# Optimization experiments

Hardware: AMD Instinct MI355X
Metric: run time of the kernel (lower is better)

## Reference

```python
import jax, jax.numpy as jnp
import numpy as np

DIM = 1024
HEADS = 16
HEAD_DIM = DIM // HEADS
MLP_HIDDEN = int(DIM * 0.7)  # 716
EPS = 1e-5


def _ln(x, g, b):
    m = jnp.mean(x, axis=-1, keepdims=True)
    v = jnp.mean(jnp.square(x - m), axis=-1, keepdims=True)
    return (x - m) * jax.lax.rsqrt(v + EPS) * g + b


def setup_inputs() -> dict:
    key = jax.random.key(0)
    ks = jax.random.split(key, 8)
    B, N = 4, 1024
    x = jax.random.normal(ks[0], (B, N, DIM), dtype=jnp.float32)
    s = 0.02
    return {
        "x": x,
        "norm_g": jnp.ones((DIM,), jnp.float32),
        "norm_b": jnp.zeros((DIM,), jnp.float32),
        "W1": jax.random.normal(ks[1], (DIM, 3 * DIM + MLP_HIDDEN), jnp.float32) * s,
        "b1": jnp.zeros((3 * DIM + MLP_HIDDEN,), jnp.float32),
        "qn_g": jnp.ones((HEAD_DIM,), jnp.float32),
        "qn_b": jnp.zeros((HEAD_DIM,), jnp.float32),
        "kn_g": jnp.ones((HEAD_DIM,), jnp.float32),
        "kn_b": jnp.zeros((HEAD_DIM,), jnp.float32),
        "projW": jax.random.normal(ks[2], (DIM, DIM), jnp.float32) * s,
        "projb": jnp.zeros((DIM,), jnp.float32),
        "mlpW": jax.random.normal(ks[3], (MLP_HIDDEN, DIM), jnp.float32) * s,  # mlp_bias=False
        "W2": jax.random.normal(ks[4], (2 * DIM, DIM), jnp.float32) * s,
        "b2": jnp.zeros((DIM,), jnp.float32),
        "ls_g": jnp.full((DIM,), 1e-5, jnp.float32),
    }


def reference(x, norm_g, norm_b, W1, b1, qn_g, qn_b, kn_g, kn_b,
              projW, projb, mlpW, W2, b2, ls_g):
    B, N, C = x.shape
    norm_x = _ln(x, norm_g, norm_b)
    f1 = norm_x @ W1 + b1  # (B, N, 3*dim + mlp_hidden)
    qkv, mlp_hidden = f1[..., :3 * DIM], f1[..., 3 * DIM:]
    # (B, N, 3, H, hd) -> (3, B, H, N, hd)
    qkv = qkv.reshape(B, N, 3, HEADS, HEAD_DIM).transpose(2, 0, 3, 1, 4)
    q, k, v = qkv[0], qkv[1], qkv[2]
    q = _ln(q, qn_g, qn_b)
    k = _ln(k, kn_g, kn_b)
    attn = jnp.einsum('bhnd,bhmd->bhnm', q, k) * (HEAD_DIM ** -0.5)
    attn = jax.nn.softmax(attn, axis=-1)
    xo = jnp.einsum('bhnm,bhmd->bhnd', attn, v)
    xo = xo.transpose(0, 2, 1, 3).reshape(B, N, DIM)
    attn_out = xo @ projW + projb
    mlp_out = jax.nn.gelu(mlp_hidden, approximate=False) @ mlpW  # no bias
    combined = jnp.concatenate([attn_out, mlp_out], axis=-1)
    out = x + (combined @ W2 + b2) * ls_g
    return out
```

## Files before the change

kernel.cpp:

```cpp
#include <hip/hip_runtime.h>
#include <cstdint>
#include <cstddef>

typedef unsigned short u16;
typedef unsigned char u8;
typedef __attribute__((ext_vector_type(8))) u16 u16x8;
typedef __attribute__((ext_vector_type(8))) __bf16 bf16x8;
typedef __attribute__((ext_vector_type(4))) float f32x4;
typedef __attribute__((ext_vector_type(16))) float f32x16;
typedef __attribute__((ext_vector_type(4))) int i32x4;
typedef __attribute__((ext_vector_type(8))) int i32x8;
typedef __attribute__((ext_vector_type(2))) int i32x2;

__device__ __forceinline__ u16 f2bf(float f) {
  unsigned u = __builtin_bit_cast(unsigned, f);
  return (u16)((u + 0x7FFFu + ((u >> 16) & 1u)) >> 16);
}
__device__ __forceinline__ float bf2f(u16 h) {
  return __builtin_bit_cast(float, (unsigned)h << 16);
}
__device__ __forceinline__ u8 f2fp8(float f) {
  return (u8)(__builtin_amdgcn_cvt_pk_fp8_f32(f, 0.f, 0, false) & 0xFF);
}
__device__ __forceinline__ f32x4 mfma16(u16x8 a, u16x8 b, f32x4 c) {
  return __builtin_amdgcn_mfma_f32_16x16x32_bf16(
      __builtin_bit_cast(bf16x8, a), __builtin_bit_cast(bf16x8, b), c, 0, 0, 0);
}
__device__ __forceinline__ f32x16 mfma32(u16x8 a, u16x8 b, f32x16 c) {
  return __builtin_amdgcn_mfma_f32_32x32x16_bf16(
      __builtin_bit_cast(bf16x8, a), __builtin_bit_cast(bf16x8, b), c, 0, 0, 0);
}
__device__ __forceinline__ unsigned cvtpk_bf16(float lo, float hi) {
  unsigned r;
  asm("v_cvt_pk_bf16_f32 %0, %1, %2" : "=v"(r) : "v"(lo), "v"(hi));
  return r;
}
__device__ __forceinline__ void plswap(unsigned& a, unsigned& b) {
  i32x2 r = __builtin_amdgcn_permlane32_swap((int)a, (int)b, false, false);
  a = (unsigned)r[0];
  b = (unsigned)r[1];
}
__device__ __forceinline__ void load_lds16(const void* g, void* l) {
  __builtin_amdgcn_global_load_lds(
      (const __attribute__((address_space(1))) void*)g,
      (__attribute__((address_space(3))) void*)l, 16, 0, 0);
}

__global__ __launch_bounds__(256) void k_pre(
    const float* __restrict__ W1, const float* __restrict__ projW,
    const float* __restrict__ mlpW, const float* __restrict__ W2,
    u8* __restrict__ W1t, u8* __restrict__ pWt, u8* __restrict__ mWt,
    u8* __restrict__ W2t, const float* __restrict__ x,
    const float* __restrict__ g, const float* __restrict__ b,
    u8* __restrict__ nx8) {
  __shared__ float t[32][33];
  __shared__ float red[8];
  const int L = blockIdx.x;
  const int tid = threadIdx.x;
  if (L < 7680) {
    const float* src;
    u8* dst;
    int R, C, dR, dC, bx, by;
    if (L < 3840) {
      src = W1; dst = W1t; R = 1024; C = 3788; dR = 1024; dC = 3840;
      bx = L % 120; by = L / 120;
    } else if (L < 4864) {
      int tq = L - 3840;
      src = projW; dst = pWt; R = 1024; C = 1024; dR = 1024; dC = 1024;
      bx = tq & 31; by = tq >> 5;
    } else if (L < 5632) {
      int tq = L - 4864;
      src = mlpW; dst = mWt; R = 716; C = 1024; dR = 768; dC = 1024;
      bx = tq & 31; by = tq >> 5;
    } else {
      int tq = L - 5632;
      src = W2; dst = W2t; R = 2048; C = 1024; dR = 2048; dC = 1024;
      bx = tq & 31; by = tq >> 5;
    }
    const int n0 = bx * 32, k0 = by * 32;
    const int tx = tid & 31, ty = tid >> 5;
#pragma unroll
    for (int j = 0; j < 4; ++j) {
      int kk = k0 + ty + 8 * j, nn = n0 + tx;
      float v = (kk < R && nn < C) ? src[(size_t)kk * C + nn] : 0.f;
      t[ty + 8 * j][tx] = v;
    }
    __syncthreads();
#pragma unroll
    for (int j = 0; j < 4; ++j) {
      int nn = n0 + ty + 8 * j, kk = k0 + tx;
      if (nn < dC && kk < dR) dst[(size_t)nn * dR + kk] = f2fp8(t[tx][ty + 8 * j]);
    }
  } else {
    const int row = L - 7680;
    float4 v = ((const float4*)(x + (size_t)row * 1024))[tid];
    float s = v.x + v.y + v.z + v.w;
    float ss = v.x * v.x + v.y * v.y + v.z * v.z + v.w * v.w;
#pragma unroll
    for (int off = 1; off < 64; off <<= 1) {
      s += __shfl_xor(s, off);
      ss += __shfl_xor(ss, off);
    }
    const int wid = tid >> 6, lane = tid & 63;
    if (lane == 0) { red[wid] = s; red[4 + wid] = ss; }
    __syncthreads();
    s = red[0] + red[1] + red[2] + red[3];
    ss = red[4] + red[5] + red[6] + red[7];
    const float mean = s * (1.f / 1024.f);
    const float var = ss * (1.f / 1024.f) - mean * mean;
    const float rstd = rsqrtf(var + 1e-5f);
    float4 gv = ((const float4*)g)[tid];
    float4 bv = ((const float4*)b)[tid];
    float y0 = (v.x - mean) * rstd * gv.x + bv.x;
    float y1 = (v.y - mean) * rstd * gv.y + bv.y;
    float y2 = (v.z - mean) * rstd * gv.z + bv.z;
    float y3 = (v.w - mean) * rstd * gv.w + bv.w;
    int pk = __builtin_amdgcn_cvt_pk_fp8_f32(y0, y1, 0, false);
    pk = __builtin_amdgcn_cvt_pk_fp8_f32(y2, y3, pk, true);
    ((int*)(nx8 + (size_t)row * 1024))[tid] = pk;
  }
}

__device__ __forceinline__ void gemm_fp8_core(const u8* __restrict__ A,
                                              const u8* __restrict__ B, int K,
                                              u8* Alds, u8* Blds,
                                              f32x16 (&acc)[2][2], int tid) {
  const int lane = tid & 63, wave = tid >> 6;
  const int h = lane >> 5, r32 = lane & 31;
  const int wrow = (wave >> 1) * 64, wcol = (wave & 1) * 64;
  const int srow0 = tid >> 2, spos = tid & 3;
  const int nk = K >> 6;
  auto STAGE = [&](int t, int bb) {
#pragma unroll
    for (int p = 0; p < 2; ++p) {
      const int row = p * 64 + srow0;
      const int c = spos ^ ((row >> 1) & 3);
      const size_t go = (size_t)row * K + (size_t)t * 64 + c * 16;
      load_lds16(A + go, Alds + bb * 8192 + (p * 256 + tid) * 16);
      load_lds16(B + go, Blds + bb * 8192 + (p * 256 + tid) * 16);
    }
  };
  STAGE(0, 0);
  STAGE(1, 1);
  asm volatile("s_waitcnt vmcnt(4)" ::: "memory");
  __builtin_amdgcn_s_barrier();
  int cur = 0;
  for (int kt = 0; kt < nk; ++kt) {
    const u8* Ac = Alds + cur * 8192;
    const u8* Bc = Blds + cur * 8192;
    i32x8 af[2], bf[2];
#pragma unroll
    for (int t = 0; t < 2; ++t) {
      {
        const int row = wrow + t * 32 + r32;
        const int sw = (row >> 1) & 3;
        i32x4 lo = *(const i32x4*)(Ac + row * 64 + ((2 * h) ^ sw) * 16);
        i32x4 hi = *(const i32x4*)(Ac + row * 64 + ((2 * h + 1) ^ sw) * 16);
        i32x8 a;
        a[0] = lo[0]; a[1] = lo[1]; a[2] = lo[2]; a[3] = lo[3];
        a[4] = hi[0]; a[5] = hi[1]; a[6] = hi[2]; a[7] = hi[3];
        af[t] = a;
      }
      {
        const int row = wcol + t * 32 + r32;
        const int sw = (row >> 1) & 3;
        i32x4 lo = *(const i32x4*)(Bc + row * 64 + ((2 * h) ^ sw) * 16);
        i32x4 hi = *(const i32x4*)(Bc + row * 64 + ((2 * h + 1) ^ sw) * 16);
        i32x8 b8;
        b8[0] = lo[0]; b8[1] = lo[1]; b8[2] = lo[2]; b8[3] = lo[3];
        b8[4] = hi[0]; b8[5] = hi[1]; b8[6] = hi[2]; b8[7] = hi[3];
        bf[t] = b8;
      }
    }
    if (kt + 2 < nk) STAGE(kt + 2, cur == 0 ? 2 : cur - 1);
#pragma unroll
    for (int i = 0; i < 2; ++i)
#pragma unroll
      for (int j = 0; j < 2; ++j)
        acc[i][j] = __builtin_amdgcn_mfma_scale_f32_32x32x64_f8f6f4(
            af[i], bf[j], acc[i][j], 0, 0, 0, 0x7F7F7F7F, 0, 0x7F7F7F7F);
    if (kt + 1 < nk) {
      if (kt + 2 < nk)
        asm volatile("s_waitcnt vmcnt(4)" ::: "memory");
      else
        asm volatile("s_waitcnt vmcnt(0)" ::: "memory");
      __builtin_amdgcn_s_barrier();
    }
    cur = (cur == 2) ? 0 : cur + 1;
  }
}

__device__ __forceinline__ void gemm_fp8_core64(const u8* __restrict__ A,
                                                const u8* __restrict__ B, int K,
                                                u8* Alds, u8* Blds,
                                                f32x16 (&acc)[2], int tid) {
  const int lane = tid & 63, wave = tid >> 6;
  const int h = lane >> 5, r32 = lane & 31;
  const int wrow = (wave >> 1) * 32, wcol = (wave & 1) * 64;
  const int nk = K >> 6;
  const int ra = tid >> 2, posa = tid & 3;
  const int ca = posa ^ ((ra >> 1) & 3);
  auto STAGE = [&](int t, int bb) {
    const size_t k0 = (size_t)t * 64;
    load_lds16(A + (size_t)ra * K + k0 + ca * 16, Alds + bb * 4096 + tid * 16);
#pragma unroll
    for (int p = 0; p < 2; ++p) {
      const int s = tid + 256 * p;
      const int r = s >> 2, pos = s & 3;
      const int c = pos ^ ((r >> 1) & 3);
      load_lds16(B + (size_t)r * K + k0 + c * 16, Blds + bb * 8192 + s * 16);
    }
  };
  STAGE(0, 0);
  STAGE(1, 1);
  asm volatile("s_waitcnt vmcnt(3)" ::: "memory");
  __builtin_amdgcn_s_barrier();
  int cur = 0;
  for (int kt = 0; kt < nk; ++kt) {
    const u8* Ac = Alds + cur * 4096;
    const u8* Bc = Blds + cur * 8192;
    i32x8 af, bf[2];
    {
      const int row = wrow + r32;
      const int sw = (row >> 1) & 3;
      i32x4 lo = *(const i32x4*)(Ac + row * 64 + ((2 * h) ^ sw) * 16);
      i32x4 hi = *(const i32x4*)(Ac + row * 64 + ((2 * h + 1) ^ sw) * 16);
      af[0] = lo[0]; af[1] = lo[1]; af[2] = lo[2]; af[3] = lo[3];
      af[4] = hi[0]; af[5] = hi[1]; af[6] = hi[2]; af[7] = hi[3];
    }
#pragma unroll
    for (int t = 0; t < 2; ++t) {
      const int row = wcol + t * 32 + r32;
      const int sw = (row >> 1) & 3;
      i32x4 lo = *(const i32x4*)(Bc + row * 64 + ((2 * h) ^ sw) * 16);
      i32x4 hi = *(const i32x4*)(Bc + row * 64 + ((2 * h + 1) ^ sw) * 16);
      i32x8 b8;
      b8[0] = lo[0]; b8[1] = lo[1]; b8[2] = lo[2]; b8[3] = lo[3];
      b8[4] = hi[0]; b8[5] = hi[1]; b8[6] = hi[2]; b8[7] = hi[3];
      bf[t] = b8;
    }
    if (kt + 2 < nk) STAGE(kt + 2, cur == 0 ? 2 : cur - 1);
#pragma unroll
    for (int j = 0; j < 2; ++j)
      acc[j] = __builtin_amdgcn_mfma_scale_f32_32x32x64_f8f6f4(
          af, bf[j], acc[j], 0, 0, 0, 0x7F7F7F7F, 0, 0x7F7F7F7F);
    if (kt + 1 < nk) {
      if (kt + 2 < nk)
        asm volatile("s_waitcnt vmcnt(3)" ::: "memory");
      else
        asm volatile("s_waitcnt vmcnt(0)" ::: "memory");
      __builtin_amdgcn_s_barrier();
    }
    cur = (cur == 2) ? 0 : cur + 1;
  }
}

__global__ __launch_bounds__(256) void k_gemm1(const u8* __restrict__ nx8,
                                               const u8* __restrict__ W1t,
                                               u16* __restrict__ f1,
                                               const float* __restrict__ b1) {
  __shared__ __align__(16) u8 Alds[3 * 128 * 64];
  __shared__ __align__(16) u8 Blds[3 * 128 * 64];
  const int tid = threadIdx.x, bm = blockIdx.y, bn = blockIdx.x;
  f32x16 acc[2][2];
#pragma unroll
  for (int i = 0; i < 2; ++i)
#pragma unroll
    for (int j = 0; j < 2; ++j)
#pragma unroll
      for (int r = 0; r < 16; ++r) acc[i][j][r] = 0.f;
  gemm_fp8_core(nx8 + (size_t)bm * 128 * 1024, W1t + (size_t)bn * 128 * 1024, 1024,
                Alds, Blds, acc, tid);
  const int lane = tid & 63, wave = tid >> 6;
  const int h = lane >> 5, r32 = lane & 31;
  const int wrow = (wave >> 1) * 64, wcol = (wave & 1) * 64;
#pragma unroll
  for (int i = 0; i < 2; ++i)
#pragma unroll
    for (int j = 0; j < 2; ++j) {
      const int col = bn * 128 + wcol + j * 32 + r32;
      const float bs = (col < 3788) ? b1[col] : 0.f;
#pragma unroll
      for (int r = 0; r < 16; ++r) {
        const int row = bm * 128 + wrow + i * 32 + 4 * h + (r & 3) + 8 * (r >> 2);
        f1[(size_t)row * 3840 + col] = f2bf(acc[i][j][r] + bs);
      }
    }
}

__global__ __launch_bounds__(256) void k_gemm_pm(
    const u8* __restrict__ xo, const u8* __restrict__ pWt,
    const u8* __restrict__ gel, const u8* __restrict__ mWt,
    u8* __restrict__ comb, const float* __restrict__ projb) {
  __shared__ __align__(16) u8 Alds[3 * 64 * 64];
  __shared__ __align__(16) u8 Blds[3 * 128 * 64];
  const int tid = threadIdx.x, bm = blockIdx.y, bnq = blockIdx.x;
  const u8* A;
  const u8* B;
  int K, colbase;
  const float* bias;
  if (bnq < 8) {
    A = xo + (size_t)bm * 64 * 1024;
    B = pWt + (size_t)bnq * 128 * 1024;
    K = 1024; colbase = bnq * 128; bias = projb;
  } else {
    A = gel + (size_t)bm * 64 * 768;
    B = mWt + (size_t)(bnq - 8) * 128 * 768;
    K = 768; colbase = 1024 + (bnq - 8) * 128; bias = nullptr;
  }
  f32x16 acc[2];
#pragma unroll
  for (int j = 0; j < 2; ++j)
#pragma unroll
    for (int r = 0; r < 16; ++r) acc[j][r] = 0.f;
  gemm_fp8_core64(A, B, K, Alds, Blds, acc, tid);
  const int lane = tid & 63, wave = tid >> 6;
  const int h = lane >> 5, r32 = lane & 31;
  const int wrow = (wave >> 1) * 32, wcol = (wave & 1) * 64;
#pragma unroll
  for (int j = 0; j < 2; ++j) {
    const int col = colbase + wcol + j * 32 + r32;
    const float bs = (bias != nullptr) ? bias[col] : 0.f;
#pragma unroll
    for (int r = 0; r < 16; ++r) {
      const int row = bm * 64 + wrow + 4 * h + (r & 3) + 8 * (r >> 2);
      comb[(size_t)row * 2048 + col] = f2fp8(acc[j][r] + bs);
    }
  }
}

__global__ __launch_bounds__(256) void k_gemm_fin(const u8* __restrict__ comb,
                                                  const u8* __restrict__ W2t,
                                                  float* __restrict__ out,
                                                  const float* __restrict__ b2,
                                                  const float* __restrict__ x,
                                                  const float* __restrict__ lsg) {
  __shared__ __align__(16) u8 Alds[3 * 64 * 64];
  __shared__ __align__(16) u8 Blds[3 * 128 * 64];
  const int tid = threadIdx.x, bm = blockIdx.y, bn = blockIdx.x;
  f32x16 acc[2];
#pragma unroll
  for (int j = 0; j < 2; ++j)
#pragma unroll
    for (int r = 0; r < 16; ++r) acc[j][r] = 0.f;
  gemm_fp8_core64(comb + (size_t)bm * 64 * 2048, W2t + (size_t)bn * 128 * 2048, 2048,
                  Alds, Blds, acc, tid);
  const int lane = tid & 63, wave = tid >> 6;
  const int h = lane >> 5, r32 = lane & 31;
  const int wrow = (wave >> 1) * 32, wcol = (wave & 1) * 64;
#pragma unroll
  for (int j = 0; j < 2; ++j) {
    const int col = bn * 128 + wcol + j * 32 + r32;
    const float bs = b2[col], ls = lsg[col];
#pragma unroll
    for (int r = 0; r < 16; ++r) {
      const int row = bm * 64 + wrow + 4 * h + (r & 3) + 8 * (r >> 2);
      out[(size_t)row * 1024 + col] =
          x[(size_t)row * 1024 + col] + (acc[j][r] + bs) * ls;
    }
  }
}

__global__ __launch_bounds__(256) void k_mid(const u16* __restrict__ f1,
                                             const float* __restrict__ qg,
                                             const float* __restrict__ qbb,
                                             const float* __restrict__ kg,
                                             const float* __restrict__ kbb,
                                             u16* __restrict__ q,
                                             u16* __restrict__ k,
                                             u8* __restrict__ gel,
                                             u16* __restrict__ vtb) {
  __shared__ u16 tt[32][33];
  const int tid = threadIdx.x;
  const int L = blockIdx.x;
  if (L < 4096) {
    const int row = L;
    const int rem = tid >> 3;
    const int which = rem >> 4, h = rem & 15;
    const int e8 = (tid & 7) * 8;
    u16x8 xv = *(const u16x8*)(f1 + (size_t)row * 3840 + which * 1024 + h * 64 + e8);
    float xf[8];
    float s1 = 0.f, s2 = 0.f;
#pragma unroll
    for (int e = 0; e < 8; ++e) {
      xf[e] = bf2f(xv[e]);
      s1 += xf[e];
      s2 += xf[e] * xf[e];
    }
#pragma unroll
    for (int off = 1; off < 8; off <<= 1) {
      s1 += __shfl_xor(s1, off);
      s2 += __shfl_xor(s2, off);
    }
    const float mean = s1 * (1.f / 64.f);
    const float var = s2 * (1.f / 64.f) - mean * mean;
    const float rstd = rsqrtf(var + 1e-5f);
    const float* g = (which == 0) ? qg : kg;
    const float* bb = (which == 0) ? qbb : kbb;
    float4 g0 = ((const float4*)g)[e8 >> 2], g1 = ((const float4*)g)[(e8 >> 2) + 1];
    float4 b0 = ((const float4*)bb)[e8 >> 2], b1 = ((const float4*)bb)[(e8 >> 2) + 1];
    float gv[8] = {g0.x, g0.y, g0.z, g0.w, g1.x, g1.y, g1.z, g1.w};
    float bv[8] = {b0.x, b0.y, b0.z, b0.w, b1.x, b1.y, b1.z, b1.w};
    u16x8 o;
#pragma unroll
    for (int e = 0; e < 8; ++e) o[e] = f2bf((xf[e] - mean) * rstd * gv[e] + bv[e]);
    const int b = row >> 10, n = row & 1023;
    u16* dst = (which == 0) ? q : k;
    *(u16x8*)(dst + ((size_t)(b * 16 + h) * 1024 + n) * 64 + e8) = o;
  } else if (L < 5632) {
    const int id = (L - 4096) * 256 + tid;
    const int row = id / 96, c8 = id - row * 96;
    u16x8 xv = *(const u16x8*)(f1 + (size_t)row * 3840 + 3072 + c8 * 8);
    float rr[8];
#pragma unroll
    for (int e = 0; e < 8; ++e) {
      const int col = c8 * 8 + e;
      rr[e] = 0.f;
      if (col < 716) {
        float xx = bf2f(xv[e]);
        rr[e] = 0.5f * xx * (1.f + erff(xx * 0.70710678118654752f));
      }
    }
    int p0 = __builtin_amdgcn_cvt_pk_fp8_f32(rr[0], rr[1], 0, false);
    p0 = __builtin_amdgcn_cvt_pk_fp8_f32(rr[2], rr[3], p0, true);
    int p1 = __builtin_amdgcn_cvt_pk_fp8_f32(rr[4], rr[5], 0, false);
    p1 = __builtin_amdgcn_cvt_pk_fp8_f32(rr[6], rr[7], p1, true);
    uint2 pk;
    pk.x = (unsigned)p0;
    pk.y = (unsigned)p1;
    *(uint2*)(gel + (size_t)row * 768 + c8 * 8) = pk;
  } else {
    const int t = L - 5632;
    const int xq = t & 1, yq = (t >> 1) & 31, z = t >> 6;
    const int b = z >> 4, h = z & 15;
    const int d0 = xq * 32, n0 = yq * 32;
    const int tx = tid & 31, ty = tid >> 5;
#pragma unroll
    for (int j = 0; j < 4; ++j)
      tt[ty + 8 * j][tx] =
          f1[(size_t)(b * 1024 + n0 + ty + 8 * j) * 3840 + 2048 + h * 64 + d0 + tx];
    __syncthreads();
#pragma unroll
    for (int j = 0; j < 4; ++j)
      vtb[(size_t)z * 65536 + (size_t)(d0 + ty + 8 * j) * 1024 + n0 + tx] =
          tt[tx][ty + 8 * j];
  }
}

__global__ __launch_bounds__(128) void k_flash(const u16* __restrict__ q,
                                               const u16* __restrict__ k,
                                               const u16* __restrict__ vt,
                                               u8* __restrict__ xo) {
  __shared__ __align__(16) u16 Kl[2][64 * 64];
  __shared__ __align__(16) u16 Vl[2][64 * 64];
  const int tid = threadIdx.x, wave = tid >> 6, lane = tid & 63;
  const int l31 = lane & 31, h = lane >> 5;
  const int L = blockIdx.x;
  const int xcd = L & 7, i = L >> 3;
  const int bh = xcd * 8 + (i & 7), qt = i >> 3;
  const int qrow0 = qt * 64 + wave * 32;
  const u16* qb = q + ((size_t)bh * 1024 + qrow0) * 64;
  const u16* kb = k + (size_t)bh * 1024 * 64;
  const u16* vb = vt + (size_t)bh * 64 * 1024;

  u16x8 qf[4];
#pragma unroll
  for (int ds = 0; ds < 4; ++ds)
    qf[ds] = *(const u16x8*)(qb + (size_t)l31 * 64 + ds * 16 + h * 8);

  f32x16 O[2];
#pragma unroll
  for (int d2 = 0; d2 < 2; ++d2)
#pragma unroll
    for (int r = 0; r < 16; ++r) O[d2][r] = 0.f;
  float lacc = 0.f;

  int sr[4], sc[4];
#pragma unroll
  for (int p = 0; p < 4; ++p) {
    const int s = tid + 128 * p;
    sr[p] = s >> 3;
    sc[p] = (s & 7) ^ (sr[p] & 7);
  }

#pragma unroll
  for (int p = 0; p < 4; ++p) {
    const int s = tid + 128 * p;
    load_lds16(kb + (size_t)sr[p] * 64 + sc[p] * 8, (u16*)Kl[0] + s * 8);
    load_lds16(vb + (size_t)sr[p] * 1024 + sc[p] * 8, (u16*)Vl[0] + s * 8);
  }
  __syncthreads();

  for (int kv = 0; kv < 16; ++kv) {
    const int cur = kv & 1;
    if (kv < 15) {
      const size_t ko = (size_t)(kv + 1) * 64;
#pragma unroll
      for (int p = 0; p < 4; ++p) {
        const int s = tid + 128 * p;
        load_lds16(kb + (ko + sr[p]) * 64 + sc[p] * 8, (u16*)Kl[cur ^ 1] + s * 8);
        load_lds16(vb + (size_t)sr[p] * 1024 + ko + sc[p] * 8,
                   (u16*)Vl[cur ^ 1] + s * 8);
      }
    }
    const u16* Kc = (const u16*)Kl[cur];
    const u16* Vc = (const u16*)Vl[cur];

    f32x16 S[2];
#pragma unroll
    for (int t2 = 0; t2 < 2; ++t2)
#pragma unroll
      for (int r = 0; r < 16; ++r) S[t2][r] = 0.f;
    __builtin_amdgcn_s_setprio(1);
#pragma unroll
    for (int t2 = 0; t2 < 2; ++t2) {
      const int kr = t2 * 32 + l31;
      const int sw = kr & 7;
#pragma unroll
      for (int ds = 0; ds < 4; ++ds) {
        const int pos = (ds * 2 + h) ^ sw;
        u16x8 kf = *(const u16x8*)(Kc + kr * 64 + pos * 8);
        S[t2] = mfma32(kf, qf[ds], S[t2]);
      }
    }
    __builtin_amdgcn_s_setprio(0);

#pragma unroll
    for (int t2 = 0; t2 < 2; ++t2)
#pragma unroll
      for (int r = 0; r < 16; ++r) {
        float pv = __expf(S[t2][r] * 0.125f);
        S[t2][r] = pv;
        lacc += pv;
      }

    __builtin_amdgcn_s_setprio(1);
#pragma unroll
    for (int m = 0; m < 4; ++m) {
      const int t2 = m >> 1, ro = (m & 1) * 8;
      unsigned w0 = cvtpk_bf16(S[t2][ro + 0], S[t2][ro + 1]);
      unsigned w2 = cvtpk_bf16(S[t2][ro + 4], S[t2][ro + 5]);
      unsigned w1 = cvtpk_bf16(S[t2][ro + 2], S[t2][ro + 3]);
      unsigned w3 = cvtpk_bf16(S[t2][ro + 6], S[t2][ro + 7]);
      plswap(w0, w2);
      plswap(w1, w3);
      i32x4 aw;
      aw[0] = (int)w0; aw[1] = (int)w1; aw[2] = (int)w2; aw[3] = (int)w3;
      const u16x8 pa = __builtin_bit_cast(u16x8, aw);
#pragma unroll
      for (int d2 = 0; d2 < 2; ++d2) {
        const int vr = d2 * 32 + l31;
        const int pos = (m * 2 + h) ^ (vr & 7);
        u16x8 vf = *(const u16x8*)(Vc + vr * 64 + pos * 8);
        O[d2] = mfma32(pa, vf, O[d2]);
      }
    }
    __builtin_amdgcn_s_setprio(0);
    __syncthreads();
  }

  lacc += __shfl_xor(lacc, 32);
  const float inv = 1.f / lacc;
  const int b = bh >> 4, hh = bh & 15;
#pragma unroll
  for (int r = 0; r < 16; ++r) {
    const int qr = (r & 3) + 8 * (r >> 2) + 4 * h;
    const float invr = __shfl(inv, qr);
    u8* orow = xo + (size_t)(b * 1024 + qrow0 + qr) * 1024 + hh * 64;
    orow[l31] = f2fp8(O[0][r] * invr);
    orow[32 + l31] = f2fp8(O[1][r] * invr);
  }
}

extern "C" void kernel_launch(void* const* d_in, const int* in_sizes, int n_in,
                              void* d_out, int out_size, void* d_ws, size_t ws_size,
                              hipStream_t stream) {
  (void)in_sizes; (void)n_in; (void)out_size; (void)ws_size;
  const float* x      = (const float*)d_in[0];
  const float* norm_g = (const float*)d_in[1];
  const float* norm_b = (const float*)d_in[2];
  const float* W1     = (const float*)d_in[3];
  const float* b1     = (const float*)d_in[4];
  const float* qn_g   = (const float*)d_in[5];
  const float* qn_b   = (const float*)d_in[6];
  const float* kn_g   = (const float*)d_in[7];
  const float* kn_b   = (const float*)d_in[8];
  const float* projW  = (const float*)d_in[9];
  const float* projb  = (const float*)d_in[10];
  const float* mlpW   = (const float*)d_in[11];
  const float* W2     = (const float*)d_in[12];
  const float* b2     = (const float*)d_in[13];
  const float* ls_g   = (const float*)d_in[14];

  char* ws = (char*)d_ws;
  u8*  W1t8 = (u8*)(ws + 0);
  u8*  pWt8 = (u8*)(ws + 3932160);
  u8*  mWt8 = (u8*)(ws + 4980736);
  u8*  W2t8 = (u8*)(ws + 5767168);
  u8*  nx8  = (u8*)(ws + 7864320);
  u16* f1   = (u16*)(ws + 12058624);
  u16* qbuf = (u16*)(ws + 43515904);
  u16* kbuf = (u16*)(ws + 51904512);
  u16* vtb  = (u16*)(ws + 60293120);
  u8*  gel8 = (u8*)(ws + 68681728);

  k_pre<<<11776, 256, 0, stream>>>(W1, projW, mlpW, W2, W1t8, pWt8, mWt8, W2t8,
                                   x, norm_g, norm_b, nx8);
  k_gemm1<<<dim3(30, 32), 256, 0, stream>>>(nx8, W1t8, f1, b1);
  k_mid<<<9728, 256, 0, stream>>>(f1, qn_g, qn_b, kn_g, kn_b, qbuf, kbuf, gel8,
                                  vtb);
  k_flash<<<1024, 128, 0, stream>>>(qbuf, kbuf, vtb, nx8);
  k_gemm_pm<<<dim3(16, 64), 256, 0, stream>>>(nx8, pWt8, gel8, mWt8, (u8*)f1, projb);
  k_gemm_fin<<<dim3(8, 64), 256, 0, stream>>>((u8*)f1, W2t8, (float*)d_out, b2, x,
                                              ls_g);
}
```

Baseline: 223.4 us.

## Restructure flash attention to single-wave blocks with 32-key tiles and vmcnt pipelining

The flash kernel now uses one wave per block (2048 blocks of 64 threads) with 32-key KV tiles, double-buffered through direct global-to-LDS loads and synchronized with explicit s_waitcnt instead of __syncthreads. K and V fragments are read from LDS into registers before the next stage is issued, with a new swizzle for the smaller tiles. The exponential becomes a raw v_exp_f32 with the scale folded into a log2e constant. The aim is to drop block barriers and raise occupancy, at the cost of more reliance on hand-placed wait counts, which could be fragile.

Result: slower. 234.0 us (+4.7%).

```diff
diff --git a/kernel.cpp b/kernel.cpp
--- a/kernel.cpp
+++ b/kernel.cpp
@@ -22,10 +22,6 @@
 __device__ __forceinline__ u8 f2fp8(float f) {
   return (u8)(__builtin_amdgcn_cvt_pk_fp8_f32(f, 0.f, 0, false) & 0xFF);
 }
-__device__ __forceinline__ f32x4 mfma16(u16x8 a, u16x8 b, f32x4 c) {
-  return __builtin_amdgcn_mfma_f32_16x16x32_bf16(
-      __builtin_bit_cast(bf16x8, a), __builtin_bit_cast(bf16x8, b), c, 0, 0, 0);
-}
 __device__ __forceinline__ f32x16 mfma32(u16x8 a, u16x8 b, f32x16 c) {
   return __builtin_amdgcn_mfma_f32_32x32x16_bf16(
       __builtin_bit_cast(bf16x8, a), __builtin_bit_cast(bf16x8, b), c, 0, 0, 0);
@@ -33,6 +29,11 @@
 __device__ __forceinline__ unsigned cvtpk_bf16(float lo, float hi) {
   unsigned r;
   asm("v_cvt_pk_bf16_f32 %0, %1, %2" : "=v"(r) : "v"(lo), "v"(hi));
+  return r;
+}
+__device__ __forceinline__ float exp2_fast(float x) {
+  float r;
+  asm("v_exp_f32 %0, %1" : "=v"(r) : "v"(x));
   return r;
 }
 __device__ __forceinline__ void plswap(unsigned& a, unsigned& b) {
@@ -447,18 +448,19 @@
   }
 }
 
-__global__ __launch_bounds__(128) void k_flash(const u16* __restrict__ q,
-                                               const u16* __restrict__ k,
-                                               const u16* __restrict__ vt,
-                                               u8* __restrict__ xo) {
-  __shared__ __align__(16) u16 Kl[2][64 * 64];
-  __shared__ __align__(16) u16 Vl[2][64 * 64];
-  const int tid = threadIdx.x, wave = tid >> 6, lane = tid & 63;
+__global__ __launch_bounds__(64) void k_flash(const u16* __restrict__ q,
+                                              const u16* __restrict__ k,
+                                              const u16* __restrict__ vt,
+                                              u8* __restrict__ xo) {
+  __shared__ __align__(16) u16 Kl[2][32 * 64];
+  __shared__ __align__(16) u16 Vl[2][64 * 32];
+  const int lane = threadIdx.x & 63;
   const int l31 = lane & 31, h = lane >> 5;
   const int L = blockIdx.x;
   const int xcd = L & 7, i = L >> 3;
-  const int bh = xcd * 8 + (i & 7), qt = i >> 3;
-  const int qrow0 = qt * 64 + wave * 32;
+  const int bh = xcd * 8 + (i & 7);
+  const int qt = i >> 3;
+  const int qrow0 = qt * 32;
   const u16* qb = q + ((size_t)bh * 1024 + qrow0) * 64;
   const u16* kb = k + (size_t)bh * 1024 * 64;
   const u16* vb = vt + (size_t)bh * 64 * 1024;
@@ -467,6 +469,7 @@
 #pragma unroll
   for (int ds = 0; ds < 4; ++ds)
     qf[ds] = *(const u16x8*)(qb + (size_t)l31 * 64 + ds * 16 + h * 8);
+  asm volatile("s_waitcnt vmcnt(0)" ::: "memory");
 
   f32x16 O[2];
 #pragma unroll
@@ -475,88 +478,78 @@
     for (int r = 0; r < 16; ++r) O[d2][r] = 0.f;
   float lacc = 0.f;
 
-  int sr[4], sc[4];
-#pragma unroll
-  for (int p = 0; p < 4; ++p) {
-    const int s = tid + 128 * p;
-    sr[p] = s >> 3;
-    sc[p] = (s & 7) ^ (sr[p] & 7);
-  }
-
-#pragma unroll
-  for (int p = 0; p < 4; ++p) {
-    const int s = tid + 128 * p;
-    load_lds16(kb + (size_t)sr[p] * 64 + sc[p] * 8, (u16*)Kl[0] + s * 8);
-    load_lds16(vb + (size_t)sr[p] * 1024 + sc[p] * 8, (u16*)Vl[0] + s * 8);
-  }
-  __syncthreads();
-
-  for (int kv = 0; kv < 16; ++kv) {
-    const int cur = kv & 1;
-    if (kv < 15) {
-      const size_t ko = (size_t)(kv + 1) * 64;
-#pragma unroll
-      for (int p = 0; p < 4; ++p) {
-        const int s = tid + 128 * p;
-        load_lds16(kb + (ko + sr[p]) * 64 + sc[p] * 8, (u16*)Kl[cur ^ 1] + s * 8);
-        load_lds16(vb + (size_t)sr[p] * 1024 + ko + sc[p] * 8,
-                   (u16*)Vl[cur ^ 1] + s * 8);
+  auto STAGE = [&](int t, int bb) {
+#pragma unroll
+    for (int p = 0; p < 4; ++p) {
+      const int s = lane + 64 * p;
+      const int kr = s >> 3, kslot = s & 7;
+      const int kc = kslot ^ ((kr ^ (kr >> 3)) & 7);
+      load_lds16(kb + (size_t)(t * 32 + kr) * 64 + kc * 8, (u16*)Kl[bb] + s * 8);
+      const int vr = s >> 2, vslot = s & 3;
+      const int vc = vslot ^ ((vr >> 1) & 3);
+      load_lds16(vb + (size_t)vr * 1024 + t * 32 + vc * 8, (u16*)Vl[bb] + s * 8);
+    }
+  };
+  STAGE(0, 0);
+  STAGE(1, 1);
+
+  const int swzk = (l31 & 7) ^ ((l31 >> 3) & 3);
+  for (int t = 0; t < 32; ++t) {
+    if (t < 31)
+      asm volatile("s_waitcnt vmcnt(8)" ::: "memory");
+    else
+      asm volatile("s_waitcnt vmcnt(0)" ::: "memory");
+    const u16* Kc = (const u16*)Kl[t & 1];
+    const u16* Vc = (const u16*)Vl[t & 1];
+    u16x8 kf[4], vf[4];
+#pragma unroll
+    for (int ds = 0; ds < 4; ++ds) {
+      const int pos = (ds * 2 + h) ^ swzk;
+      kf[ds] = *(const u16x8*)(Kc + l31 * 64 + pos * 8);
+    }
+#pragma unroll
+    for (int m = 0; m < 2; ++m)
+#pragma unroll
+      for (int d2 = 0; d2 < 2; ++d2) {
+        const int vr = d2 * 32 + l31;
+        const int pos = (m * 2 + h) ^ ((vr >> 1) & 3);
+        vf[m * 2 + d2] = *(const u16x8*)(Vc + vr * 32 + pos * 8);
       }
-    }
-    const u16* Kc = (const u16*)Kl[cur];
-    const u16* Vc = (const u16*)Vl[cur];
-
-    f32x16 S[2];
-#pragma unroll
-    for (int t2 = 0; t2 < 2; ++t2)
-#pragma unroll
-      for (int r = 0; r < 16; ++r) S[t2][r] = 0.f;
+    asm volatile("s_waitcnt lgkmcnt(0)" ::: "memory");
+    if (t + 2 < 32) STAGE(t + 2, t & 1);
+
+    f32x16 S;
+#pragma unroll
+    for (int r = 0; r < 16; ++r) S[r] = 0.f;
     __builtin_amdgcn_s_setprio(1);
 #pragma unroll
-    for (int t2 = 0; t2 < 2; ++t2) {
-      const int kr = t2 * 32 + l31;
-      const int sw = kr & 7;
-#pragma unroll
-      for (int ds = 0; ds < 4; ++ds) {
-        const int pos = (ds * 2 + h) ^ sw;
-        u16x8 kf = *(const u16x8*)(Kc + kr * 64 + pos * 8);
-        S[t2] = mfma32(kf, qf[ds], S[t2]);
-      }
-    }
+    for (int ds = 0; ds < 4; ++ds) S = mfma32(kf[ds], qf[ds], S);
     __builtin_amdgcn_s_setprio(0);
 
 #pragma unroll
-    for (int t2 = 0; t2 < 2; ++t2)
-#pragma unroll
-      for (int r = 0; r < 16; ++r) {
-        float pv = __expf(S[t2][r] * 0.125f);
-        S[t2][r] = pv;
-        lacc += pv;
-      }
+    for (int r = 0; r < 16; ++r) {
+      float pv = exp2_fast(S[r] * 0.18033688011112042f);
+      S[r] = pv;
+      lacc += pv;
+    }
 
     __builtin_amdgcn_s_setprio(1);
 #pragma unroll
-    for (int m = 0; m < 4; ++m) {
-      const int t2 = m >> 1, ro = (m & 1) * 8;
-      unsigned w0 = cvtpk_bf16(S[t2][ro + 0], S[t2][ro + 1]);
-      unsigned w2 = cvtpk_bf16(S[t2][ro + 4], S[t2][ro + 5]);
-      unsigned w1 = cvtpk_bf16(S[t2][ro + 2], S[t2][ro + 3]);
-      unsigned w3 = cvtpk_bf16(S[t2][ro + 6], S[t2][ro + 7]);
+    for (int m = 0; m < 2; ++m) {
+      const int ro = m * 8;
+      unsigned w0 = cvtpk_bf16(S[ro + 0], S[ro + 1]);
+      unsigned w2 = cvtpk_bf16(S[ro + 4], S[ro + 5]);
+      unsigned w1 = cvtpk_bf16(S[ro + 2], S[ro + 3]);
+      unsigned w3 = cvtpk_bf16(S[ro + 6], S[ro + 7]);
       plswap(w0, w2);
       plswap(w1, w3);
       i32x4 aw;
       aw[0] = (int)w0; aw[1] = (int)w1; aw[2] = (int)w2; aw[3] = (int)w3;
       const u16x8 pa = __builtin_bit_cast(u16x8, aw);
 #pragma unroll
-      for (int d2 = 0; d2 < 2; ++d2) {
-        const int vr = d2 * 32 + l31;
-        const int pos = (m * 2 + h) ^ (vr & 7);
-        u16x8 vf = *(const u16x8*)(Vc + vr * 64 + pos * 8);
-        O[d2] = mfma32(pa, vf, O[d2]);
-      }
+      for (int d2 = 0; d2 < 2; ++d2) O[d2] = mfma32(pa, vf[m * 2 + d2], O[d2]);
     }
     __builtin_amdgcn_s_setprio(0);
-    __syncthreads();
   }
 
   lacc += __shfl_xor(lacc, 32);
@@ -609,7 +602,7 @@
   k_gemm1<<<dim3(30, 32), 256, 0, stream>>>(nx8, W1t8, f1, b1);
   k_mid<<<9728, 256, 0, stream>>>(f1, qn_g, qn_b, kn_g, kn_b, qbuf, kbuf, gel8,
                                   vtb);
-  k_flash<<<1024, 128, 0, stream>>>(qbuf, kbuf, vtb, nx8);
+  k_flash<<<2048, 64, 0, stream>>>(qbuf, kbuf, vtb, nx8);
   k_gemm_pm<<<dim3(16, 64), 256, 0, stream>>>(nx8, pWt8, gel8, mWt8, (u8*)f1, projb);
   k_gemm_fin<<<dim3(8, 64), 256, 0, stream>>>((u8*)f1, W2t8, (float*)d_out, b2, x,
                                               ls_g);
```
